# Kernel optimization log

Hardware: AMD Instinct MI355X
Metric: run time of the kernel (lower is better)

Reference implementation:

```python
import jax, jax.numpy as jnp
import numpy as np
import math

B, I, H = 8192, 1024, 1024

def _uniform(key, shape, lo, hi):
    return jax.random.uniform(key, shape, dtype=jnp.float32, minval=lo, maxval=hi)

def setup_inputs() -> dict:
    key = jax.random.key(0)
    ks = jax.random.split(key, 14)
    bound = math.sqrt(1.0 / H)
    lo, hi = -bound, bound
    x = jax.random.normal(ks[0], (B, I), dtype=jnp.float32)
    hid = jax.random.normal(ks[1], (B, H), dtype=jnp.float32)
    # stacked params for gates [r, z, n]
    wx = jnp.stack([_uniform(ks[2 + i], (I, H), lo, hi) for i in range(3)])   # [3, I, H]
    wh = jnp.stack([_uniform(ks[5 + i], (H, H), lo, hi) for i in range(3)])   # [3, H, H]
    bx = jnp.stack([_uniform(ks[8 + i], (H,), lo, hi) for i in range(3)])     # [3, H]
    bh = jnp.stack([_uniform(ks[11 + i], (H,), lo, hi) for i in range(3)])    # [3, H]
    return {"x": x, "hid": hid, "wx": wx, "wh": wh, "bx": bx, "bh": bh}

def reference(x, hid, wx, wh, bx, bh):
    # Fused gate projections: one big matmul per source instead of 3 small ones.
    gx = jnp.einsum('bi,gih->bgh', x, wx) + bx[None]        # [B, 3, H]
    gh = jnp.einsum('bh,ghk->bgk', hid, wh) + bh[None]      # [B, 3, H]
    r = jax.nn.sigmoid(gx[:, 0] + gh[:, 0])
    z = jax.nn.sigmoid(gx[:, 1] + gh[:, 1])
    n = jnp.tanh(gx[:, 2] + r * gh[:, 2])
    next_hid = (1.0 - z) * n + z * hid
    return next_hid
```

## Files before the change

kernel.cpp:

```cpp
#include <hip/hip_runtime.h>
#include <hip/hip_bf16.h>

typedef __hip_bfloat16 bf16;
typedef unsigned short u16;
typedef __attribute__((ext_vector_type(8))) short bf16x8;
typedef __attribute__((ext_vector_type(4))) float f32x4;
typedef __attribute__((ext_vector_type(8))) unsigned short u16x8;

#define KD 1024
#define HD 1024
#define BSZ 8192
#define BM 128
#define BN 64
#define BK 32

#define WS_XB 12582912
#define WS_HB 29360128
#define WS_NEED 46137344ULL

__device__ __forceinline__ u16 f2b(float f) {
    return __builtin_bit_cast(u16, __float2bfloat16(f));
}

__device__ __forceinline__ void gload16(const void* g, u16* smem, int lds_byte_off) {
    __builtin_amdgcn_global_load_lds(
        (const __attribute__((address_space(1))) void*)g,
        (__attribute__((address_space(3))) void*)((char*)smem + lds_byte_off),
        16, 0, 0);
}

__global__ __launch_bounds__(256) void convert_xh(
    const float* __restrict__ x, const float* __restrict__ h,
    u16* __restrict__ xb, u16* __restrict__ hb)
{
    size_t off = ((size_t)blockIdx.x * 256 + threadIdx.x) * 8;
    float4 a0 = *(const float4*)(x + off);
    float4 a1 = *(const float4*)(x + off + 4);
    float4 b0 = *(const float4*)(h + off);
    float4 b1 = *(const float4*)(h + off + 4);
    u16x8 vx, vh;
    vx[0]=f2b(a0.x); vx[1]=f2b(a0.y); vx[2]=f2b(a0.z); vx[3]=f2b(a0.w);
    vx[4]=f2b(a1.x); vx[5]=f2b(a1.y); vx[6]=f2b(a1.z); vx[7]=f2b(a1.w);
    vh[0]=f2b(b0.x); vh[1]=f2b(b0.y); vh[2]=f2b(b0.z); vh[3]=f2b(b0.w);
    vh[4]=f2b(b1.x); vh[5]=f2b(b1.y); vh[6]=f2b(b1.z); vh[7]=f2b(b1.w);
    *(u16x8*)(xb + off) = vx;
    *(u16x8*)(hb + off) = vh;
}

__global__ __launch_bounds__(256) void transpose_w(
    const float* __restrict__ wx, const float* __restrict__ wh, u16* __restrict__ wt)
{
    __shared__ u16 tile[64][65];
    const int g = blockIdx.z;
    const float* src = (g < 3) ? (wx + (size_t)g * KD * HD) : (wh + (size_t)(g - 3) * KD * HD);
    u16* dst = wt + (size_t)g * KD * HD;
    const int r0 = blockIdx.y * 64;
    const int c0 = blockIdx.x * 64;
    const int t = threadIdx.x;

    #pragma unroll
    for (int r = 0; r < 2; r++) {
        int idx = r * 256 + t;
        int row = idx >> 3, cc = idx & 7;
        const float* p = src + (size_t)(r0 + row) * HD + c0 + cc * 8;
        #pragma unroll
        for (int e = 0; e < 8; e++) tile[row][cc * 8 + e] = f2b(p[e]);
    }
    __syncthreads();
    #pragma unroll
    for (int r = 0; r < 2; r++) {
        int idx = r * 256 + t;
        int nrow = idx >> 3, kc = idx & 7;
        u16x8 v;
        #pragma unroll
        for (int e = 0; e < 8; e++) v[e] = tile[kc * 8 + e][nrow];
        *(u16x8*)(dst + (size_t)(c0 + nrow) * KD + r0 + kc * 8) = v;
    }
}

__device__ __forceinline__ void gru_epilogue(
    f32x4 (&acc)[4][4][2], const float* __restrict__ bxf, const float* __restrict__ bhf,
    const float* __restrict__ hidf, float* __restrict__ outf,
    int m0, int n0, int wm, int wn, int quad, int c16)
{
    float bR[2], bZ[2], bXN[2], bHN[2];
    #pragma unroll
    for (int j = 0; j < 2; j++) {
        int col = n0 + wn * 32 + j * 16 + c16;
        bR[j]  = bxf[col]          + bhf[col];
        bZ[j]  = bxf[HD + col]     + bhf[HD + col];
        bXN[j] = bxf[2 * HD + col];
        bHN[j] = bhf[2 * HD + col];
    }
    #pragma unroll
    for (int i = 0; i < 4; i++)
        #pragma unroll
        for (int j = 0; j < 2; j++) {
            int col = n0 + wn * 32 + j * 16 + c16;
            #pragma unroll
            for (int r = 0; r < 4; r++) {
                int row = m0 + wm * 64 + i * 16 + quad * 4 + r;
                size_t idx = (size_t)row * HD + col;
                float vr = acc[0][i][j][r] + bR[j];
                vr = 1.f / (1.f + __expf(-vr));
                float vz = acc[1][i][j][r] + bZ[j];
                vz = 1.f / (1.f + __expf(-vz));
                float vn = (acc[2][i][j][r] + bXN[j]) + vr * (acc[3][i][j][r] + bHN[j]);
                float e2 = __expf(2.f * vn);
                vn = 1.f - 2.f / (e2 + 1.f);
                float o = (1.f - vz) * vn + vz * hidf[idx];
                outf[idx] = o;
            }
        }
}

__global__ __launch_bounds__(256, 2) void gru_fused_fast(
    const u16* __restrict__ xb, const u16* __restrict__ hb,
    const u16* __restrict__ wt,
    const float* __restrict__ bxf, const float* __restrict__ bhf,
    const float* __restrict__ hidf, float* __restrict__ outf)
{
    __shared__ u16 smem[20480];
    const int t    = threadIdx.x;
    const int lane = t & 63;
    const int w    = t >> 6;
    const int wm   = w >> 1, wn = w & 1;
    const int quad = lane >> 4;
    const int c16  = lane & 15;
    const int lin  = blockIdx.x;
    const int nblk = (lin & 7) * 2 + ((lin >> 3) & 1);
    const int mblk = lin >> 4;
    const int m0   = mblk * BM;
    const int n0   = nblk * BN;

    const int row4 = t >> 2;
    const int e8   = (t & 3) * 8;
    const u16* gx0 = xb + (size_t)(m0 + row4) * KD + e8;
    const u16* gx1 = gx0 + (size_t)64 * KD;
    const u16* gh0 = hb + (size_t)(m0 + row4) * KD + e8;
    const u16* gh1 = gh0 + (size_t)64 * KD;
    const u16* gw0 = wt + (size_t)(n0 + row4) * KD + e8;
    const int ldsl = w * 1024;

    f32x4 acc[4][4][2];
    #pragma unroll
    for (int a = 0; a < 4; a++)
        #pragma unroll
        for (int i = 0; i < 4; i++)
            #pragma unroll
            for (int j = 0; j < 2; j++)
                acc[a][i][j] = (f32x4){0.f, 0.f, 0.f, 0.f};

    for (int k0 = 0; k0 < KD; k0 += BK) {
        gload16(gx0, smem, ldsl);
        gload16(gx1, smem, 4096 + ldsl);
        gload16(gh0, smem, 8192 + ldsl);
        gload16(gh1, smem, 12288 + ldsl);
        #pragma unroll
        for (int g = 0; g < 6; g++)
            gload16(gw0 + (size_t)g * KD * HD, smem, 16384 + g * 4096 + ldsl);
        __syncthreads();
        gx0 += BK; gx1 += BK; gh0 += BK; gh1 += BK; gw0 += BK;

        bf16x8 ax[4], ah[4];
        #pragma unroll
        for (int i = 0; i < 4; i++) {
            int ml = wm * 64 + i * 16 + c16;
            ax[i] = *(const bf16x8*)&smem[ml * BK + quad * 8];
            ah[i] = *(const bf16x8*)&smem[4096 + ml * BK + quad * 8];
        }
        #pragma unroll
        for (int p = 0; p < 3; p++) {
            bf16x8 bwx[2], bwh[2];
            #pragma unroll
            for (int j = 0; j < 2; j++) {
                int nl = wn * 32 + j * 16 + c16;
                bwx[j] = *(const bf16x8*)&smem[8192 + p * 2048       + nl * BK + quad * 8];
                bwh[j] = *(const bf16x8*)&smem[8192 + (p + 3) * 2048 + nl * BK + quad * 8];
            }
            #pragma unroll
            for (int i = 0; i < 4; i++)
                #pragma unroll
                for (int j = 0; j < 2; j++) {
                    if (p < 2) {
                        acc[p][i][j] = __builtin_amdgcn_mfma_f32_16x16x32_bf16(ax[i], bwx[j], acc[p][i][j], 0, 0, 0);
                        acc[p][i][j] = __builtin_amdgcn_mfma_f32_16x16x32_bf16(ah[i], bwh[j], acc[p][i][j], 0, 0, 0);
                    } else {
                        acc[2][i][j] = __builtin_amdgcn_mfma_f32_16x16x32_bf16(ax[i], bwx[j], acc[2][i][j], 0, 0, 0);
                        acc[3][i][j] = __builtin_amdgcn_mfma_f32_16x16x32_bf16(ah[i], bwh[j], acc[3][i][j], 0, 0, 0);
                    }
                }
        }
        __syncthreads();
    }

    gru_epilogue(acc, bxf, bhf, hidf, outf, m0, n0, wm, wn, quad, c16);
}

__global__ __launch_bounds__(256, 2) void gru_fused_slow(
    const float* __restrict__ xf, const float* __restrict__ hf,
    const u16* __restrict__ wt,
    const float* __restrict__ bxf, const float* __restrict__ bhf,
    float* __restrict__ outf)
{
    __shared__ u16 smem[20480];
    const int t    = threadIdx.x;
    const int lane = t & 63;
    const int w    = t >> 6;
    const int wm   = w >> 1, wn = w & 1;
    const int quad = lane >> 4;
    const int c16  = lane & 15;
    const int lin  = blockIdx.x;
    const int nblk = (lin & 7) * 2 + ((lin >> 3) & 1);
    const int mblk = lin >> 4;
    const int m0   = mblk * BM;
    const int n0   = nblk * BN;
    const int row4 = t >> 2;
    const int e8   = (t & 3) * 8;
    const u16* gw0 = wt + (size_t)(n0 + row4) * KD + e8;
    const int ldsl = w * 1024;

    f32x4 acc[4][4][2];
    #pragma unroll
    for (int a = 0; a < 4; a++)
        #pragma unroll
        for (int i = 0; i < 4; i++)
            #pragma unroll
            for (int j = 0; j < 2; j++)
                acc[a][i][j] = (f32x4){0.f, 0.f, 0.f, 0.f};

    for (int k0 = 0; k0 < KD; k0 += BK) {
        #pragma unroll
        for (int g = 0; g < 6; g++)
            gload16(gw0 + (size_t)g * KD * HD, smem, 16384 + g * 4096 + ldsl);
        gw0 += BK;
        #pragma unroll
        for (int s = 0; s < 2; s++) {
            size_t gidx = (size_t)(m0 + s * 64 + row4) * KD + k0 + e8;
            const float* px = xf + gidx;
            const float* ph = hf + gidx;
            u16x8 vx, vh;
            #pragma unroll
            for (int e = 0; e < 8; e++) { vx[e] = f2b(px[e]); vh[e] = f2b(ph[e]); }
            *(u16x8*)&smem[s * 2048 + t * 8] = vx;
            *(u16x8*)&smem[4096 + s * 2048 + t * 8] = vh;
        }
        __syncthreads();

        bf16x8 ax[4], ah[4];
        #pragma unroll
        for (int i = 0; i < 4; i++) {
            int ml = wm * 64 + i * 16 + c16;
            ax[i] = *(const bf16x8*)&smem[ml * BK + quad * 8];
            ah[i] = *(const bf16x8*)&smem[4096 + ml * BK + quad * 8];
        }
        #pragma unroll
        for (int p = 0; p < 3; p++) {
            bf16x8 bwx[2], bwh[2];
            #pragma unroll
            for (int j = 0; j < 2; j++) {
                int nl = wn * 32 + j * 16 + c16;
                bwx[j] = *(const bf16x8*)&smem[8192 + p * 2048       + nl * BK + quad * 8];
                bwh[j] = *(const bf16x8*)&smem[8192 + (p + 3) * 2048 + nl * BK + quad * 8];
            }
            #pragma unroll
            for (int i = 0; i < 4; i++)
                #pragma unroll
                for (int j = 0; j < 2; j++) {
                    if (p < 2) {
                        acc[p][i][j] = __builtin_amdgcn_mfma_f32_16x16x32_bf16(ax[i], bwx[j], acc[p][i][j], 0, 0, 0);
                        acc[p][i][j] = __builtin_amdgcn_mfma_f32_16x16x32_bf16(ah[i], bwh[j], acc[p][i][j], 0, 0, 0);
                    } else {
                        acc[2][i][j] = __builtin_amdgcn_mfma_f32_16x16x32_bf16(ax[i], bwx[j], acc[2][i][j], 0, 0, 0);
                        acc[3][i][j] = __builtin_amdgcn_mfma_f32_16x16x32_bf16(ah[i], bwh[j], acc[3][i][j], 0, 0, 0);
                    }
                }
        }
        __syncthreads();
    }

    gru_epilogue(acc, bxf, bhf, hf, outf, m0, n0, wm, wn, quad, c16);
}

extern "C" void kernel_launch(void* const* d_in, const int* in_sizes, int n_in,
                              void* d_out, int out_size, void* d_ws, size_t ws_size,
                              hipStream_t stream) {
    const float* x   = (const float*)d_in[0];
    const float* hid = (const float*)d_in[1];
    const float* wx  = (const float*)d_in[2];
    const float* wh  = (const float*)d_in[3];
    const float* bx  = (const float*)d_in[4];
    const float* bh  = (const float*)d_in[5];
    float* out = (float*)d_out;

    char* ws = (char*)d_ws;
    u16* wt = (u16*)ws;
    u16* xb = (u16*)(ws + WS_XB);
    u16* hb = (u16*)(ws + WS_HB);

    dim3 tgrid(HD / 64, KD / 64, 6);
    transpose_w<<<tgrid, 256, 0, stream>>>(wx, wh, wt);

    if (ws_size >= WS_NEED) {
        convert_xh<<<4096, 256, 0, stream>>>(x, hid, xb, hb);
        gru_fused_fast<<<1024, 256, 0, stream>>>(xb, hb, wt, bx, bh, hid, out);
    } else {
        gru_fused_slow<<<1024, 256, 0, stream>>>(x, hid, wt, bx, bh, out);
    }
}
```

Baseline: 254.5 us.

## Switch to 32x32x16 MFMA with XOR-swizzled LDS layout and merged prep kernel

The main GEMM loop now uses 32x32x16 bf16 MFMA tiles instead of 16x16x32, cutting the number of LDS fragment reads per MFMA and the instruction count. Operands are pre-swizzled in global memory with an XOR pattern on the K8 chunk index so that the direct global-to-LDS loads land in a bank-conflict-reduced layout. The weight transpose and the x/h bf16 conversion are merged into one prep launch, and the LDS-tiled transpose is replaced by strided direct reads. The fallback slow path for small workspaces is removed, so the code now assumes the workspace is always large enough.

```diff
diff --git a/kernel.cpp b/kernel.cpp
--- a/kernel.cpp
+++ b/kernel.cpp
@@ -4,7 +4,7 @@
 typedef __hip_bfloat16 bf16;
 typedef unsigned short u16;
 typedef __attribute__((ext_vector_type(8))) short bf16x8;
-typedef __attribute__((ext_vector_type(4))) float f32x4;
+typedef __attribute__((ext_vector_type(16))) float f32x16;
 typedef __attribute__((ext_vector_type(8))) unsigned short u16x8;
 
 #define KD 1024
@@ -16,7 +16,6 @@
 
 #define WS_XB 12582912
 #define WS_HB 29360128
-#define WS_NEED 46137344ULL
 
 __device__ __forceinline__ u16 f2b(float f) {
     return __builtin_bit_cast(u16, __float2bfloat16(f));
@@ -29,89 +28,45 @@
         16, 0, 0);
 }
 
-__global__ __launch_bounds__(256) void convert_xh(
+__global__ __launch_bounds__(256) void prep_all(
     const float* __restrict__ x, const float* __restrict__ h,
-    u16* __restrict__ xb, u16* __restrict__ hb)
+    const float* __restrict__ wx, const float* __restrict__ wh,
+    u16* __restrict__ xb, u16* __restrict__ hb, u16* __restrict__ wtp)
 {
-    size_t off = ((size_t)blockIdx.x * 256 + threadIdx.x) * 8;
-    float4 a0 = *(const float4*)(x + off);
-    float4 a1 = *(const float4*)(x + off + 4);
-    float4 b0 = *(const float4*)(h + off);
-    float4 b1 = *(const float4*)(h + off + 4);
-    u16x8 vx, vh;
-    vx[0]=f2b(a0.x); vx[1]=f2b(a0.y); vx[2]=f2b(a0.z); vx[3]=f2b(a0.w);
-    vx[4]=f2b(a1.x); vx[5]=f2b(a1.y); vx[6]=f2b(a1.z); vx[7]=f2b(a1.w);
-    vh[0]=f2b(b0.x); vh[1]=f2b(b0.y); vh[2]=f2b(b0.z); vh[3]=f2b(b0.w);
-    vh[4]=f2b(b1.x); vh[5]=f2b(b1.y); vh[6]=f2b(b1.z); vh[7]=f2b(b1.w);
-    *(u16x8*)(xb + off) = vx;
-    *(u16x8*)(hb + off) = vh;
-}
-
-__global__ __launch_bounds__(256) void transpose_w(
-    const float* __restrict__ wx, const float* __restrict__ wh, u16* __restrict__ wt)
-{
-    __shared__ u16 tile[64][65];
-    const int g = blockIdx.z;
-    const float* src = (g < 3) ? (wx + (size_t)g * KD * HD) : (wh + (size_t)(g - 3) * KD * HD);
-    u16* dst = wt + (size_t)g * KD * HD;
-    const int r0 = blockIdx.y * 64;
-    const int c0 = blockIdx.x * 64;
-    const int t = threadIdx.x;
-
-    #pragma unroll
-    for (int r = 0; r < 2; r++) {
-        int idx = r * 256 + t;
-        int row = idx >> 3, cc = idx & 7;
-        const float* p = src + (size_t)(r0 + row) * HD + c0 + cc * 8;
-        #pragma unroll
-        for (int e = 0; e < 8; e++) tile[row][cc * 8 + e] = f2b(p[e]);
-    }
-    __syncthreads();
-    #pragma unroll
-    for (int r = 0; r < 2; r++) {
-        int idx = r * 256 + t;
-        int nrow = idx >> 3, kc = idx & 7;
+    int b = blockIdx.x;
+    if (b < 3072) {
+        int cid = b * 256 + threadIdx.x;
+        int n    = cid & 1023;
+        int rest = cid >> 10;
+        int K8   = rest & 127;
+        int g    = rest >> 7;
+        const float* src = (g < 3) ? (wx + (size_t)g * KD * HD)
+                                   : (wh + (size_t)(g - 3) * KD * HD);
         u16x8 v;
         #pragma unroll
-        for (int e = 0; e < 8; e++) v[e] = tile[kc * 8 + e][nrow];
-        *(u16x8*)(dst + (size_t)(c0 + nrow) * KD + r0 + kc * 8) = v;
-    }
-}
-
-__device__ __forceinline__ void gru_epilogue(
-    f32x4 (&acc)[4][4][2], const float* __restrict__ bxf, const float* __restrict__ bhf,
-    const float* __restrict__ hidf, float* __restrict__ outf,
-    int m0, int n0, int wm, int wn, int quad, int c16)
-{
-    float bR[2], bZ[2], bXN[2], bHN[2];
-    #pragma unroll
-    for (int j = 0; j < 2; j++) {
-        int col = n0 + wn * 32 + j * 16 + c16;
-        bR[j]  = bxf[col]          + bhf[col];
-        bZ[j]  = bxf[HD + col]     + bhf[HD + col];
-        bXN[j] = bxf[2 * HD + col];
-        bHN[j] = bhf[2 * HD + col];
-    }
-    #pragma unroll
-    for (int i = 0; i < 4; i++)
-        #pragma unroll
-        for (int j = 0; j < 2; j++) {
-            int col = n0 + wn * 32 + j * 16 + c16;
-            #pragma unroll
-            for (int r = 0; r < 4; r++) {
-                int row = m0 + wm * 64 + i * 16 + quad * 4 + r;
-                size_t idx = (size_t)row * HD + col;
-                float vr = acc[0][i][j][r] + bR[j];
-                vr = 1.f / (1.f + __expf(-vr));
-                float vz = acc[1][i][j][r] + bZ[j];
-                vz = 1.f / (1.f + __expf(-vz));
-                float vn = (acc[2][i][j][r] + bXN[j]) + vr * (acc[3][i][j][r] + bHN[j]);
-                float e2 = __expf(2.f * vn);
-                vn = 1.f - 2.f / (e2 + 1.f);
-                float o = (1.f - vz) * vn + vz * hidf[idx];
-                outf[idx] = o;
-            }
-        }
+        for (int e = 0; e < 8; e++)
+            v[e] = f2b(src[(size_t)(K8 * 8 + e) * HD + n]);
+        int K8d = (K8 & ~3) | ((K8 & 3) ^ ((n >> 1) & 3));
+        *(u16x8*)(wtp + (size_t)g * KD * HD + (size_t)n * KD + K8d * 8) = v;
+    } else {
+        int cid = (b - 3072) * 256 + threadIdx.x;
+        int row = cid >> 7;
+        int K8  = cid & 127;
+        int K8d = (K8 & ~3) | ((K8 & 3) ^ ((row >> 1) & 3));
+        size_t so = (size_t)cid * 8;
+        size_t dO = (size_t)row * KD + K8d * 8;
+        float4 a0 = *(const float4*)(x + so);
+        float4 a1 = *(const float4*)(x + so + 4);
+        float4 b0 = *(const float4*)(h + so);
+        float4 b1 = *(const float4*)(h + so + 4);
+        u16x8 vx, vh;
+        vx[0]=f2b(a0.x); vx[1]=f2b(a0.y); vx[2]=f2b(a0.z); vx[3]=f2b(a0.w);
+        vx[4]=f2b(a1.x); vx[5]=f2b(a1.y); vx[6]=f2b(a1.z); vx[7]=f2b(a1.w);
+        vh[0]=f2b(b0.x); vh[1]=f2b(b0.y); vh[2]=f2b(b0.z); vh[3]=f2b(b0.w);
+        vh[4]=f2b(b1.x); vh[5]=f2b(b1.y); vh[6]=f2b(b1.z); vh[7]=f2b(b1.w);
+        *(u16x8*)(xb + dO) = vx;
+        *(u16x8*)(hb + dO) = vh;
+    }
 }
 
 __global__ __launch_bounds__(256, 2) void gru_fused_fast(
@@ -121,12 +76,12 @@
     const float* __restrict__ hidf, float* __restrict__ outf)
 {
     __shared__ u16 smem[20480];
-    const int t    = threadIdx.x;
-    const int lane = t & 63;
-    const int w    = t >> 6;
-    const int wm   = w >> 1, wn = w & 1;
-    const int quad = lane >> 4;
-    const int c16  = lane & 15;
+    const int t     = threadIdx.x;
+    const int lane  = t & 63;
+    const int w     = t >> 6;
+    const int wm    = w >> 1, wn = w & 1;
+    const int l31   = lane & 31;
+    const int khalf = lane >> 5;
     const int lin  = blockIdx.x;
     const int nblk = (lin & 7) * 2 + ((lin >> 3) & 1);
     const int mblk = lin >> 4;
@@ -142,14 +97,35 @@
     const u16* gw0 = wt + (size_t)(n0 + row4) * KD + e8;
     const int ldsl = w * 1024;
 
-    f32x4 acc[4][4][2];
+    f32x16 acc[4][2];
     #pragma unroll
     for (int a = 0; a < 4; a++)
         #pragma unroll
-        for (int i = 0; i < 4; i++)
-            #pragma unroll
-            for (int j = 0; j < 2; j++)
-                acc[a][i][j] = (f32x4){0.f, 0.f, 0.f, 0.f};
+        for (int m = 0; m < 2; m++)
+            #pragma unroll
+            for (int r = 0; r < 16; r++)
+                acc[a][m][r] = 0.f;
+
+    int aoff[2][2], woff[2];
+    #pragma unroll
+    for (int m = 0; m < 2; m++) {
+        int R = wm * 64 + m * 32 + l31;
+        int s = (R >> 1) & 3;
+        #pragma unroll
+        for (int kk = 0; kk < 2; kk++) {
+            int q = kk * 2 + khalf;
+            aoff[m][kk] = R * 32 + ((q ^ s) * 8);
+        }
+    }
+    {
+        int nl = wn * 32 + l31;
+        int s = (nl >> 1) & 3;
+        #pragma unroll
+        for (int kk = 0; kk < 2; kk++) {
+            int q = kk * 2 + khalf;
+            woff[kk] = 8192 + nl * 32 + ((q ^ s) * 8);
+        }
+    }
 
     for (int k0 = 0; k0 < KD; k0 += BK) {
         gload16(gx0, smem, ldsl);
@@ -162,124 +138,58 @@
         __syncthreads();
         gx0 += BK; gx1 += BK; gh0 += BK; gh1 += BK; gw0 += BK;
 
-        bf16x8 ax[4], ah[4];
-        #pragma unroll
-        for (int i = 0; i < 4; i++) {
-            int ml = wm * 64 + i * 16 + c16;
-            ax[i] = *(const bf16x8*)&smem[ml * BK + quad * 8];
-            ah[i] = *(const bf16x8*)&smem[4096 + ml * BK + quad * 8];
-        }
+        bf16x8 ax[2][2], ah[2][2];
+        #pragma unroll
+        for (int m = 0; m < 2; m++)
+            #pragma unroll
+            for (int kk = 0; kk < 2; kk++) {
+                ax[m][kk] = *(const bf16x8*)&smem[aoff[m][kk]];
+                ah[m][kk] = *(const bf16x8*)&smem[4096 + aoff[m][kk]];
+            }
         #pragma unroll
         for (int p = 0; p < 3; p++) {
             bf16x8 bwx[2], bwh[2];
             #pragma unroll
-            for (int j = 0; j < 2; j++) {
-                int nl = wn * 32 + j * 16 + c16;
-                bwx[j] = *(const bf16x8*)&smem[8192 + p * 2048       + nl * BK + quad * 8];
-                bwh[j] = *(const bf16x8*)&smem[8192 + (p + 3) * 2048 + nl * BK + quad * 8];
+            for (int kk = 0; kk < 2; kk++) {
+                bwx[kk] = *(const bf16x8*)&smem[woff[kk] + p * 2048];
+                bwh[kk] = *(const bf16x8*)&smem[woff[kk] + (p + 3) * 2048];
             }
             #pragma unroll
-            for (int i = 0; i < 4; i++)
+            for (int m = 0; m < 2; m++)
                 #pragma unroll
-                for (int j = 0; j < 2; j++) {
+                for (int kk = 0; kk < 2; kk++) {
                     if (p < 2) {
-                        acc[p][i][j] = __builtin_amdgcn_mfma_f32_16x16x32_bf16(ax[i], bwx[j], acc[p][i][j], 0, 0, 0);
-                        acc[p][i][j] = __builtin_amdgcn_mfma_f32_16x16x32_bf16(ah[i], bwh[j], acc[p][i][j], 0, 0, 0);
+                        acc[p][m] = __builtin_amdgcn_mfma_f32_32x32x16_bf16(ax[m][kk], bwx[kk], acc[p][m], 0, 0, 0);
+                        acc[p][m] = __builtin_amdgcn_mfma_f32_32x32x16_bf16(ah[m][kk], bwh[kk], acc[p][m], 0, 0, 0);
                     } else {
-                        acc[2][i][j] = __builtin_amdgcn_mfma_f32_16x16x32_bf16(ax[i], bwx[j], acc[2][i][j], 0, 0, 0);
-                        acc[3][i][j] = __builtin_amdgcn_mfma_f32_16x16x32_bf16(ah[i], bwh[j], acc[3][i][j], 0, 0, 0);
+                        acc[2][m] = __builtin_amdgcn_mfma_f32_32x32x16_bf16(ax[m][kk], bwx[kk], acc[2][m], 0, 0, 0);
+                        acc[3][m] = __builtin_amdgcn_mfma_f32_32x32x16_bf16(ah[m][kk], bwh[kk], acc[3][m], 0, 0, 0);
                     }
                 }
         }
         __syncthreads();
     }
 
-    gru_epilogue(acc, bxf, bhf, hidf, outf, m0, n0, wm, wn, quad, c16);
-}
-
-__global__ __launch_bounds__(256, 2) void gru_fused_slow(
-    const float* __restrict__ xf, const float* __restrict__ hf,
-    const u16* __restrict__ wt,
-    const float* __restrict__ bxf, const float* __restrict__ bhf,
-    float* __restrict__ outf)
-{
-    __shared__ u16 smem[20480];
-    const int t    = threadIdx.x;
-    const int lane = t & 63;
-    const int w    = t >> 6;
-    const int wm   = w >> 1, wn = w & 1;
-    const int quad = lane >> 4;
-    const int c16  = lane & 15;
-    const int lin  = blockIdx.x;
-    const int nblk = (lin & 7) * 2 + ((lin >> 3) & 1);
-    const int mblk = lin >> 4;
-    const int m0   = mblk * BM;
-    const int n0   = nblk * BN;
-    const int row4 = t >> 2;
-    const int e8   = (t & 3) * 8;
-    const u16* gw0 = wt + (size_t)(n0 + row4) * KD + e8;
-    const int ldsl = w * 1024;
-
-    f32x4 acc[4][4][2];
+    const int col = n0 + wn * 32 + l31;
+    const float bR  = bxf[col]          + bhf[col];
+    const float bZ  = bxf[HD + col]     + bhf[HD + col];
+    const float bXN = bxf[2 * HD + col];
+    const float bHN = bhf[2 * HD + col];
     #pragma unroll
-    for (int a = 0; a < 4; a++)
-        #pragma unroll
-        for (int i = 0; i < 4; i++)
-            #pragma unroll
-            for (int j = 0; j < 2; j++)
-                acc[a][i][j] = (f32x4){0.f, 0.f, 0.f, 0.f};
-
-    for (int k0 = 0; k0 < KD; k0 += BK) {
-        #pragma unroll
-        for (int g = 0; g < 6; g++)
-            gload16(gw0 + (size_t)g * KD * HD, smem, 16384 + g * 4096 + ldsl);
-        gw0 += BK;
-        #pragma unroll
-        for (int s = 0; s < 2; s++) {
-            size_t gidx = (size_t)(m0 + s * 64 + row4) * KD + k0 + e8;
-            const float* px = xf + gidx;
-            const float* ph = hf + gidx;
-            u16x8 vx, vh;
-            #pragma unroll
-            for (int e = 0; e < 8; e++) { vx[e] = f2b(px[e]); vh[e] = f2b(ph[e]); }
-            *(u16x8*)&smem[s * 2048 + t * 8] = vx;
-            *(u16x8*)&smem[4096 + s * 2048 + t * 8] = vh;
-        }
-        __syncthreads();
-
-        bf16x8 ax[4], ah[4];
-        #pragma unroll
-        for (int i = 0; i < 4; i++) {
-            int ml = wm * 64 + i * 16 + c16;
-            ax[i] = *(const bf16x8*)&smem[ml * BK + quad * 8];
-            ah[i] = *(const bf16x8*)&smem[4096 + ml * BK + quad * 8];
-        }
-        #pragma unroll
-        for (int p = 0; p < 3; p++) {
-            bf16x8 bwx[2], bwh[2];
-            #pragma unroll
-            for (int j = 0; j < 2; j++) {
-                int nl = wn * 32 + j * 16 + c16;
-                bwx[j] = *(const bf16x8*)&smem[8192 + p * 2048       + nl * BK + quad * 8];
-                bwh[j] = *(const bf16x8*)&smem[8192 + (p + 3) * 2048 + nl * BK + quad * 8];
-            }
-            #pragma unroll
-            for (int i = 0; i < 4; i++)
-                #pragma unroll
-                for (int j = 0; j < 2; j++) {
-                    if (p < 2) {
-                        acc[p][i][j] = __builtin_amdgcn_mfma_f32_16x16x32_bf16(ax[i], bwx[j], acc[p][i][j], 0, 0, 0);
-                        acc[p][i][j] = __builtin_amdgcn_mfma_f32_16x16x32_bf16(ah[i], bwh[j], acc[p][i][j], 0, 0, 0);
-                    } else {
-                        acc[2][i][j] = __builtin_amdgcn_mfma_f32_16x16x32_bf16(ax[i], bwx[j], acc[2][i][j], 0, 0, 0);
-                        acc[3][i][j] = __builtin_amdgcn_mfma_f32_16x16x32_bf16(ah[i], bwh[j], acc[3][i][j], 0, 0, 0);
-                    }
-                }
-        }
-        __syncthreads();
-    }
-
-    gru_epilogue(acc, bxf, bhf, hf, outf, m0, n0, wm, wn, quad, c16);
+    for (int m = 0; m < 2; m++)
+        #pragma unroll
+        for (int r = 0; r < 16; r++) {
+            int row = m0 + wm * 64 + m * 32 + (r & 3) + 8 * (r >> 2) + 4 * khalf;
+            size_t idx = (size_t)row * HD + col;
+            float vr = acc[0][m][r] + bR;
+            vr = 1.f / (1.f + __expf(-vr));
+            float vz = acc[1][m][r] + bZ;
+            vz = 1.f / (1.f + __expf(-vz));
+            float vn = (acc[2][m][r] + bXN) + vr * (acc[3][m][r] + bHN);
+            float e2 = __expf(2.f * vn);
+            vn = 1.f - 2.f / (e2 + 1.f);
+            outf[idx] = (1.f - vz) * vn + vz * hidf[idx];
+        }
 }
 
 extern "C" void kernel_launch(void* const* d_in, const int* in_sizes, int n_in,
@@ -298,13 +208,6 @@
     u16* xb = (u16*)(ws + WS_XB);
     u16* hb = (u16*)(ws + WS_HB);
 
-    dim3 tgrid(HD / 64, KD / 64, 6);
-    transpose_w<<<tgrid, 256, 0, stream>>>(wx, wh, wt);
-
-    if (ws_size >= WS_NEED) {
-        convert_xh<<<4096, 256, 0, stream>>>(x, hid, xb, hb);
-        gru_fused_fast<<<1024, 256, 0, stream>>>(xb, hb, wt, bx, bh, hid, out);
-    } else {
-        gru_fused_slow<<<1024, 256, 0, stream>>>(x, hid, wt, bx, bh, out);
-    }
-}
+    prep_all<<<7168, 256, 0, stream>>>(x, hid, wx, wh, xb, hb, wt);
+    gru_fused_fast<<<1024, 256, 0, stream>>>(xb, hb, wt, bx, bh, hid, out);
+}
```

Measured after the change: 259.3 us. No clear change (+1.9%).
